# Performance work log

Measured on AMD Instinct MI355X. Metric: run time of the kernel, lower is better.

The kernel has to match this reference:

```python
import jax, jax.numpy as jnp
import numpy as np

N = 100000
E = 1600000
IN_C, HID_C, OUT_C = 128, 256, 40


def sage_conv(x, src, dst, W_l, W_r, b):
    # mean aggregation of source-node features into destination nodes
    msgs = x[src]                                            # [E, d]
    agg = jax.ops.segment_sum(msgs, dst, num_segments=N)     # [N, d]
    deg = jax.ops.segment_sum(jnp.ones((src.shape[0],), x.dtype), dst,
                              num_segments=N)                # [N]
    agg = agg / jnp.clip(deg, 1.0, None)[:, None]
    # out = lin_l(agg) + lin_r(x); weights stored [out, in] like torch
    return agg @ W_l.T + x @ W_r.T + b


def setup_inputs() -> dict:
    key = jax.random.key(0)
    ks = jax.random.split(key, 10)
    s = 0.05
    x = jax.random.normal(ks[0], (N, IN_C), dtype=jnp.float32)
    edge_index = jax.random.randint(ks[1], (2, E), 0, N, dtype=jnp.int64)
    return {
        "x": x,
        "edge_index": edge_index,
        "W_l0": jax.random.normal(ks[2], (HID_C, IN_C), dtype=jnp.float32) * s,
        "W_r0": jax.random.normal(ks[3], (HID_C, IN_C), dtype=jnp.float32) * s,
        "b0": jnp.zeros((HID_C,), jnp.float32),
        "W_l1": jax.random.normal(ks[4], (HID_C, HID_C), dtype=jnp.float32) * s,
        "W_r1": jax.random.normal(ks[5], (HID_C, HID_C), dtype=jnp.float32) * s,
        "b1": jnp.zeros((HID_C,), jnp.float32),
        "W_lo": jax.random.normal(ks[6], (OUT_C, HID_C), dtype=jnp.float32) * s,
        "W_ro": jax.random.normal(ks[7], (OUT_C, HID_C), dtype=jnp.float32) * s,
        "bo": jnp.zeros((OUT_C,), jnp.float32),
    }


def reference(x, edge_index, W_l0, W_r0, b0, W_l1, W_r1, b1, W_lo, W_ro, bo):
    src, dst = edge_index[0], edge_index[1]
    h = jax.nn.relu(sage_conv(x, src, dst, W_l0, W_r0, b0))
    h = jax.nn.relu(sage_conv(h, src, dst, W_l1, W_r1, b1))
    out = sage_conv(h, src, dst, W_lo, W_ro, bo)
    return jax.nn.log_softmax(out, axis=1)
```

## Files before the change

### kernel.cpp

```cpp
#include <hip/hip_runtime.h>
#include <hip/hip_bf16.h>
#include <cstdint>
#include <cstddef>

#define NN   100000
#define NE   1600000
#define HID  256
#define OUTC 40

typedef __attribute__((ext_vector_type(8))) short bf16x8;
typedef __attribute__((ext_vector_type(4))) float f32x4;

static __device__ __forceinline__ ushort f2bf(float f) {
    __hip_bfloat16 h = __float2bfloat16(f);
    return *reinterpret_cast<ushort*>(&h);
}
static __device__ __forceinline__ float bflo(unsigned u) { return __uint_as_float(u << 16); }
static __device__ __forceinline__ float bfhi(unsigned u) { return __uint_as_float(u & 0xffff0000u); }
static __device__ __forceinline__ float ubf(unsigned w, int k) {
    return (float)((w >> (8 * k)) & 255u);
}

__global__ void k_count(const int* __restrict__ dst, int* __restrict__ cnt) {
    int i = blockIdx.x * blockDim.x + threadIdx.x;
    if (i < NE) atomicAdd(&cnt[dst[i]], 1);
}

__global__ void k_blocksum(const int* __restrict__ cnt, int* __restrict__ bsum) {
    __shared__ int s[256];
    int t = threadIdx.x;
    int n = blockIdx.x * 256 + t;
    s[t] = (n < NN) ? cnt[n] : 0;
    __syncthreads();
    for (int off = 128; off; off >>= 1) {
        if (t < off) s[t] += s[t + off];
        __syncthreads();
    }
    if (t == 0) bsum[blockIdx.x] = s[0];
}

__global__ void k_scanblock(const int* __restrict__ bsum, int* __restrict__ boff, int nb) {
    __shared__ int s[512];
    int t = threadIdx.x;
    int v = (t < nb) ? bsum[t] : 0;
    s[t] = v;
    __syncthreads();
    for (int off = 1; off < 512; off <<= 1) {
        int u = (t >= off) ? s[t - off] : 0;
        __syncthreads();
        s[t] += u;
        __syncthreads();
    }
    if (t < nb) boff[t] = s[t] - v;
}

__global__ void k_rowptr(const int* __restrict__ cnt, const int* __restrict__ boff,
                         int* __restrict__ rowptr, int* __restrict__ fillp,
                         float* __restrict__ invd) {
    __shared__ int s[256];
    int t = threadIdx.x;
    int n = blockIdx.x * 256 + t;
    int c = (n < NN) ? cnt[n] : 0;
    s[t] = c;
    __syncthreads();
    for (int off = 1; off < 256; off <<= 1) {
        int u = (t >= off) ? s[t - off] : 0;
        __syncthreads();
        s[t] += u;
        __syncthreads();
    }
    if (n < NN) {
        int excl = boff[blockIdx.x] + s[t] - c;
        rowptr[n] = excl;
        fillp[n]  = excl;
        invd[n]   = 1.0f / (float)(c > 1 ? c : 1);
    }
    if (n == 0) rowptr[NN] = NE;
}

__global__ void k_fill(const int* __restrict__ src, const int* __restrict__ dst,
                       int* __restrict__ fillp, int* __restrict__ colidx) {
    int i = blockIdx.x * blockDim.x + threadIdx.x;
    if (i < NE) {
        int p = atomicAdd(&fillp[dst[i]], 1);
        colidx[p] = src[i];
    }
}

__global__ void k_cvtfrag(const float* __restrict__ W, ushort* __restrict__ dst,
                          int ocreal, int d, int nf) {
    int f = blockIdx.x * 256 + threadIdx.x;
    if (f >= nf) return;
    int lm = f & 15, lk = (f >> 4) & 3;
    int rest = f >> 6;
    int dk = d / 32;
    int kk = rest % dk, cc = rest / dk;
    int row = cc * 16 + lm, col = kk * 32 + lk * 8;
    unsigned q0 = 0, q1 = 0, q2 = 0, q3 = 0;
    if (row < ocreal) {
        const float4* p = (const float4*)(W + (size_t)row * d + col);
        float4 a = p[0], b = p[1];
        q0 = (unsigned)f2bf(a.x) | ((unsigned)f2bf(a.y) << 16);
        q1 = (unsigned)f2bf(a.z) | ((unsigned)f2bf(a.w) << 16);
        q2 = (unsigned)f2bf(b.x) | ((unsigned)f2bf(b.y) << 16);
        q3 = (unsigned)f2bf(b.z) | ((unsigned)f2bf(b.w) << 16);
    }
    *(uint4*)(dst + (size_t)f * 8) = make_uint4(q0, q1, q2, q3);
}

__global__ __launch_bounds__(256) void k_quant_x8(const float* __restrict__ x,
                                                  unsigned char* __restrict__ xq,
                                                  float* __restrict__ sx) {
    int t = threadIdx.x;
    int qw = t >> 4, ql = t & 15;
    int row = blockIdx.x * 16 + qw;
    if (row >= NN) return;
    const float4* p = (const float4*)(x + (size_t)row * 128 + ql * 8);
    float4 a = p[0], b = p[1];
    float v[8] = {a.x, a.y, a.z, a.w, b.x, b.y, b.z, b.w};
    float m = 0.f;
    #pragma unroll
    for (int k = 0; k < 8; ++k) m = fmaxf(m, fabsf(v[k]));
    m = fmaxf(m, __shfl_xor(m, 1));
    m = fmaxf(m, __shfl_xor(m, 2));
    m = fmaxf(m, __shfl_xor(m, 4));
    m = fmaxf(m, __shfl_xor(m, 8));
    float inv = (m > 0.f) ? 127.f / m : 0.f;
    unsigned w0 = 0, w1 = 0;
    #pragma unroll
    for (int k = 0; k < 4; ++k)
        w0 |= ((unsigned)((int)rintf(v[k] * inv) + 128) & 255u) << (8 * k);
    #pragma unroll
    for (int k = 0; k < 4; ++k)
        w1 |= ((unsigned)((int)rintf(v[4 + k] * inv) + 128) & 255u) << (8 * k);
    *(uint2*)(xq + (size_t)row * 128 + ql * 8) = make_uint2(w0, w1);
    if (ql == 0) sx[row] = (m > 0.f) ? m / 127.f : 0.f;
}

__global__ __launch_bounds__(256, 3) void k_layer0(
    const unsigned char* __restrict__ xq, const float* __restrict__ sx,
    const float* __restrict__ xf,
    const ushort* __restrict__ Wl, const ushort* __restrict__ Wr,
    const float* __restrict__ bias, const float* __restrict__ invd,
    const int* __restrict__ rowptr, const int* __restrict__ colidx,
    unsigned char* __restrict__ hq, float* __restrict__ hs)
{
    __shared__ ushort aggS[64 * 128];
    __shared__ int cidxS[2048];
    char* aggSb = (char*)aggS;
    const int t  = threadIdx.x;
    const int r0 = blockIdx.x * 64;
    const int l = t & 63;

    const int ebase = rowptr[r0];
    const int rend  = (r0 + 64 < NN) ? (r0 + 64) : NN;
    const int etot  = rowptr[rend] - ebase;
    const bool inlds = (etot <= 2048);
    if (inlds) {
        for (int i = t; i < etot; i += 256) cidxS[i] = colidx[ebase + i];
    }
    __syncthreads();

    {
        const int gid = t >> 3, li = t & 7;
        const int base = l & ~7;
        for (int rr = gid; rr < 64; rr += 32) {
            const int r = r0 + rr;
            float acc[16];
            #pragma unroll
            for (int k = 0; k < 16; ++k) acc[k] = 0.f;
            float sum_sc = 0.f;
            if (r < NN) {
                const int beg = rowptr[r], end = rowptr[r + 1];
                for (int e = beg; e < end; e += 8) {
                    const int myi = e + li;
                    int se = -1;
                    if (myi < end) se = inlds ? cidxS[myi - ebase] : colidx[myi];
                    float mysc = (se >= 0) ? sx[se] : 0.f;
                    int   sj[8];
                    float sc[8];
                    uint4 u[8];
                    #pragma unroll
                    for (int j = 0; j < 8; ++j) sj[j] = __shfl(se, base + j);
                    #pragma unroll
                    for (int j = 0; j < 8; ++j) sc[j] = __shfl(mysc, base + j);
                    #pragma unroll
                    for (int j = 0; j < 8; ++j) {
                        u[j] = (sj[j] >= 0)
                            ? *(const uint4*)(xq + (((unsigned)sj[j]) << 7) + (li << 4))
                            : make_uint4(0u, 0u, 0u, 0u);
                    }
                    #pragma unroll
                    for (int j = 0; j < 8; ++j) {
                        #pragma unroll
                        for (int wi = 0; wi < 4; ++wi) {
                            unsigned w = (&u[j].x)[wi];
                            acc[wi*4+0] = fmaf(sc[j], ubf(w, 0), acc[wi*4+0]);
                            acc[wi*4+1] = fmaf(sc[j], ubf(w, 1), acc[wi*4+1]);
                            acc[wi*4+2] = fmaf(sc[j], ubf(w, 2), acc[wi*4+2]);
                            acc[wi*4+3] = fmaf(sc[j], ubf(w, 3), acc[wi*4+3]);
                        }
                        sum_sc += sc[j];
                    }
                }
                const float iv = invd[r];
                #pragma unroll
                for (int k = 0; k < 16; ++k) acc[k] = (acc[k] - 128.f * sum_sc) * iv;
            }
            #pragma unroll
            for (int gg = 0; gg < 2; ++gg) {
                unsigned q0 = (unsigned)f2bf(acc[gg*8+0]) | ((unsigned)f2bf(acc[gg*8+1]) << 16);
                unsigned q1 = (unsigned)f2bf(acc[gg*8+2]) | ((unsigned)f2bf(acc[gg*8+3]) << 16);
                unsigned q2 = (unsigned)f2bf(acc[gg*8+4]) | ((unsigned)f2bf(acc[gg*8+5]) << 16);
                unsigned q3 = (unsigned)f2bf(acc[gg*8+6]) | ((unsigned)f2bf(acc[gg*8+7]) << 16);
                int g  = li * 2 + gg;
                int gs = g ^ (rr & 7);
                *(uint4*)(aggSb + (size_t)rr * 256 + (gs << 4)) = make_uint4(q0, q1, q2, q3);
            }
        }
    }
    __syncthreads();

    const int w = t >> 6, lm = l & 15, lk = l >> 4;
    const int rr = w * 16 + lm;
    const int rg = r0 + rr;

    bf16x8 ax[4];
    #pragma unroll
    for (int kk = 0; kk < 4; ++kk) {
        bf16x8 v;
        if (rg < NN) {
            const float4* p = (const float4*)(xf + (size_t)rg * 128 + kk * 32 + lk * 8);
            float4 f0 = p[0], f1 = p[1];
            v[0] = (short)f2bf(f0.x); v[1] = (short)f2bf(f0.y);
            v[2] = (short)f2bf(f0.z); v[3] = (short)f2bf(f0.w);
            v[4] = (short)f2bf(f1.x); v[5] = (short)f2bf(f1.y);
            v[6] = (short)f2bf(f1.z); v[7] = (short)f2bf(f1.w);
        } else v = (bf16x8)(short)0;
        ax[kk] = v;
    }

    f32x4 acc[16];
    #pragma unroll
    for (int cc = 0; cc < 16; ++cc) acc[cc] = {0.f, 0.f, 0.f, 0.f};

    #pragma unroll
    for (int kk = 0; kk < 4; ++kk) {
        int g  = kk * 4 + lk;
        int gs = g ^ (rr & 7);
        bf16x8 a_agg = *(const bf16x8*)(aggSb + (size_t)rr * 256 + (gs << 4));
        #pragma unroll
        for (int cc = 0; cc < 16; ++cc) {
            const size_t wf = ((size_t)(cc * 4 + kk) * 64 + l) * 8;
            bf16x8 bl = *(const bf16x8*)(Wl + wf);
            bf16x8 br = *(const bf16x8*)(Wr + wf);
            acc[cc] = __builtin_amdgcn_mfma_f32_16x16x32_bf16(a_agg,  bl, acc[cc], 0, 0, 0);
            acc[cc] = __builtin_amdgcn_mfma_f32_16x16x32_bf16(ax[kk], br, acc[cc], 0, 0, 0);
        }
    }

    float vmax[4] = {0.f, 0.f, 0.f, 0.f};
    #pragma unroll
    for (int cc = 0; cc < 16; ++cc) {
        const float bv = bias[cc * 16 + lm];
        #pragma unroll
        for (int i = 0; i < 4; ++i) {
            float v = fmaxf(acc[cc][i] + bv, 0.f);
            acc[cc][i] = v;
            vmax[i] = fmaxf(vmax[i], v);
        }
    }
    #pragma unroll
    for (int i = 0; i < 4; ++i) {
        vmax[i] = fmaxf(vmax[i], __shfl_xor(vmax[i], 1));
        vmax[i] = fmaxf(vmax[i], __shfl_xor(vmax[i], 2));
        vmax[i] = fmaxf(vmax[i], __shfl_xor(vmax[i], 4));
        vmax[i] = fmaxf(vmax[i], __shfl_xor(vmax[i], 8));
    }
    float invq[4];
    #pragma unroll
    for (int i = 0; i < 4; ++i) invq[i] = (vmax[i] > 0.f) ? 255.f / vmax[i] : 0.f;
    const int ob = r0 + w * 16 + lk * 4;
    if (lm == 0) {
        #pragma unroll
        for (int i = 0; i < 4; ++i)
            if (ob + i < NN) hs[ob + i] = vmax[i] / 255.f;
    }
    #pragma unroll
    for (int cc = 0; cc < 16; ++cc) {
        #pragma unroll
        for (int i = 0; i < 4; ++i) {
            if (ob + i < NN)
                hq[(size_t)(ob + i) * 256 + cc * 16 + lm] =
                    (unsigned char)(int)rintf(acc[cc][i] * invq[i]);
        }
    }
}

__global__ __launch_bounds__(256, 3) void k_layer1(
    const unsigned char* __restrict__ hq, const float* __restrict__ hs,
    const ushort* __restrict__ Wl, const ushort* __restrict__ Wr,
    const float* __restrict__ bias,
    const ushort* __restrict__ wlo, const ushort* __restrict__ wro,
    const float* __restrict__ bo,
    const float* __restrict__ invd,
    const int* __restrict__ rowptr, const int* __restrict__ colidx,
    unsigned char* __restrict__ qq, float* __restrict__ sq, float* __restrict__ rbuf)
{
    __shared__ ushort aggS[64 * 256];
    __shared__ int cidxS[2048];
    char* aggSb = (char*)aggS;
    const int t  = threadIdx.x;
    const int r0 = blockIdx.x * 64;
    const int l = t & 63;

    const int ebase = rowptr[r0];
    const int rend  = (r0 + 64 < NN) ? (r0 + 64) : NN;
    const int etot  = rowptr[rend] - ebase;
    const bool inlds = (etot <= 2048);
    if (inlds) {
        for (int i = t; i < etot; i += 256) cidxS[i] = colidx[ebase + i];
    }
    __syncthreads();

    {
        const int gid = t >> 4, li = t & 15;
        const int base = l & ~15;
        for (int rr = gid; rr < 64; rr += 16) {
            const int r = r0 + rr;
            float acc[16];
            #pragma unroll
            for (int k = 0; k < 16; ++k) acc[k] = 0.f;
            if (r < NN) {
                const int beg = rowptr[r], end = rowptr[r + 1];
                for (int e = beg; e < end; e += 8) {
                    const int myi = e + (li & 7);
                    int se = -1;
                    if (myi < end) se = inlds ? cidxS[myi - ebase] : colidx[myi];
                    float mysc = (se >= 0) ? hs[se] : 0.f;
                    int   sj[8];
                    float sc[8];
                    uint4 u[8];
                    #pragma unroll
                    for (int j = 0; j < 8; ++j) sj[j] = __shfl(se, base + j);
                    #pragma unroll
                    for (int j = 0; j < 8; ++j) sc[j] = __shfl(mysc, base + j);
                    #pragma unroll
                    for (int j = 0; j < 8; ++j) {
                        u[j] = (sj[j] >= 0)
                            ? *(const uint4*)(hq + (((unsigned)sj[j]) << 8) + (li << 4))
                            : make_uint4(0u, 0u, 0u, 0u);
                    }
                    #pragma unroll
                    for (int j = 0; j < 8; ++j) {
                        #pragma unroll
                        for (int wi = 0; wi < 4; ++wi) {
                            unsigned w = (&u[j].x)[wi];
                            acc[wi*4+0] = fmaf(sc[j], ubf(w, 0), acc[wi*4+0]);
                            acc[wi*4+1] = fmaf(sc[j], ubf(w, 1), acc[wi*4+1]);
                            acc[wi*4+2] = fmaf(sc[j], ubf(w, 2), acc[wi*4+2]);
                            acc[wi*4+3] = fmaf(sc[j], ubf(w, 3), acc[wi*4+3]);
                        }
                    }
                }
                const float iv = invd[r];
                #pragma unroll
                for (int k = 0; k < 16; ++k) acc[k] *= iv;
            }
            #pragma unroll
            for (int gg = 0; gg < 2; ++gg) {
                unsigned q0 = (unsigned)f2bf(acc[gg*8+0]) | ((unsigned)f2bf(acc[gg*8+1]) << 16);
                unsigned q1 = (unsigned)f2bf(acc[gg*8+2]) | ((unsigned)f2bf(acc[gg*8+3]) << 16);
                unsigned q2 = (unsigned)f2bf(acc[gg*8+4]) | ((unsigned)f2bf(acc[gg*8+5]) << 16);
                unsigned q3 = (unsigned)f2bf(acc[gg*8+6]) | ((unsigned)f2bf(acc[gg*8+7]) << 16);
                int g  = li * 2 + gg;
                int gs = g ^ (rr & 7);
                *(uint4*)(aggSb + (size_t)rr * 512 + (gs << 4)) = make_uint4(q0, q1, q2, q3);
            }
        }
    }
    __syncthreads();

    const int w = t >> 6, lm = l & 15, lk = l >> 4;
    const int rr = w * 16 + lm;
    const int rg = r0 + rr;

    bf16x8 ax[8];
    {
        const float sr = (rg < NN) ? hs[rg] : 0.f;
        #pragma unroll
        for (int kk = 0; kk < 8; ++kk) {
            uint2 uq = (rg < NN)
                ? *(const uint2*)(hq + (((unsigned)rg) << 8) + kk * 32 + lk * 8)
                : make_uint2(0u, 0u);
            bf16x8 v;
            v[0] = (short)f2bf(sr * ubf(uq.x, 0));
            v[1] = (short)f2bf(sr * ubf(uq.x, 1));
            v[2] = (short)f2bf(sr * ubf(uq.x, 2));
            v[3] = (short)f2bf(sr * ubf(uq.x, 3));
            v[4] = (short)f2bf(sr * ubf(uq.y, 0));
            v[5] = (short)f2bf(sr * ubf(uq.y, 1));
            v[6] = (short)f2bf(sr * ubf(uq.y, 2));
            v[7] = (short)f2bf(sr * ubf(uq.y, 3));
            ax[kk] = v;
        }
    }

    f32x4 acc[16];
    #pragma unroll
    for (int cc = 0; cc < 16; ++cc) acc[cc] = {0.f, 0.f, 0.f, 0.f};

    #pragma unroll
    for (int kk = 0; kk < 8; ++kk) {
        int g  = kk * 4 + lk;
        int gs = g ^ (rr & 7);
        bf16x8 a_agg = *(const bf16x8*)(aggSb + (size_t)rr * 512 + (gs << 4));
        #pragma unroll
        for (int cc = 0; cc < 16; ++cc) {
            const size_t wf = ((size_t)(cc * 8 + kk) * 64 + l) * 8;
            bf16x8 bl = *(const bf16x8*)(Wl + wf);
            bf16x8 br = *(const bf16x8*)(Wr + wf);
            acc[cc] = __builtin_amdgcn_mfma_f32_16x16x32_bf16(a_agg,  bl, acc[cc], 0, 0, 0);
            acc[cc] = __builtin_amdgcn_mfma_f32_16x16x32_bf16(ax[kk], br, acc[cc], 0, 0, 0);
        }
    }

    #pragma unroll
    for (int cc = 0; cc < 16; ++cc) {
        const int c = cc * 16 + lm;
        const float bv = bias[c];
        #pragma unroll
        for (int i = 0; i < 4; ++i) {
            float v = fmaxf(acc[cc][i] + bv, 0.f);
            int row = w * 16 + lk * 4 + i;
            int g = c >> 3;
            int gs = g ^ (row & 7);
            *(ushort*)(aggSb + (size_t)row * 512 + (gs << 4) + ((c & 7) << 1)) = f2bf(v);
        }
    }
    __syncthreads();

    f32x4 aq[3], ar[3];
    #pragma unroll
    for (int cc = 0; cc < 3; ++cc) { aq[cc] = {0.f,0.f,0.f,0.f}; ar[cc] = {0.f,0.f,0.f,0.f}; }

    const int prow = w * 16 + lm;
    #pragma unroll
    for (int kk = 0; kk < 8; ++kk) {
        int g  = kk * 4 + lk;
        int gs = g ^ (prow & 7);
        bf16x8 a = *(const bf16x8*)(aggSb + (size_t)prow * 512 + (gs << 4));
        #pragma unroll
        for (int cc = 0; cc < 3; ++cc) {
            const size_t wf = ((size_t)(cc * 8 + kk) * 64 + l) * 8;
            bf16x8 bl = *(const bf16x8*)(wlo + wf);
            bf16x8 br = *(const bf16x8*)(wro + wf);
            aq[cc] = __builtin_amdgcn_mfma_f32_16x16x32_bf16(a, bl, aq[cc], 0, 0, 0);
            ar[cc] = __builtin_amdgcn_mfma_f32_16x16x32_bf16(a, br, ar[cc], 0, 0, 0);
        }
    }

    #pragma unroll
    for (int i = 0; i < 4; ++i) {
        const int orow = r0 + w * 16 + lk * 4 + i;
        if (orow >= NN) continue;
        float m = 0.f;
        #pragma unroll
        for (int cc = 0; cc < 3; ++cc) {
            const int c = cc * 16 + lm;
            if (c < OUTC) m = fmaxf(m, fabsf(aq[cc][i]));
        }
        m = fmaxf(m, __shfl_xor(m, 1));
        m = fmaxf(m, __shfl_xor(m, 2));
        m = fmaxf(m, __shfl_xor(m, 4));
        m = fmaxf(m, __shfl_xor(m, 8));
        const float inv = (m > 0.f) ? 127.f / m : 0.f;
        #pragma unroll
        for (int cc = 0; cc < 3; ++cc) {
            const int c = cc * 16 + lm;
            int code = (c < OUTC) ? (int)rintf(aq[cc][i] * inv) : 0;
            qq[(size_t)orow * 64 + c] = (unsigned char)(code + 128);
            rbuf[(size_t)orow * 64 + c] = (c < OUTC) ? (ar[cc][i] + bo[c]) : 0.f;
        }
        qq[(size_t)orow * 64 + 48 + lm] = (unsigned char)128;
        rbuf[(size_t)orow * 64 + 48 + lm] = 0.f;
        if (lm == 0) sq[orow] = m / 127.f;
    }
}

__global__ __launch_bounds__(256) void k_final(
    const unsigned char* __restrict__ qq, const float* __restrict__ sq,
    const float* __restrict__ rbuf, const float* __restrict__ invd,
    const int* __restrict__ rowptr, const int* __restrict__ colidx,
    float* __restrict__ out)
{
    __shared__ int cidxS[2048];
    const int t = threadIdx.x;
    const int g = t >> 2, li = t & 3;
    const int r0 = blockIdx.x * 64;
    const int row = r0 + g;
    const int l = t & 63;
    const int base = l & ~3;

    const int ebase = rowptr[r0];
    const int rend  = (r0 + 64 < NN) ? (r0 + 64) : NN;
    const int etot  = rowptr[rend] - ebase;
    const bool inlds = (etot <= 2048);
    if (inlds) {
        for (int i = t; i < etot; i += 256) cidxS[i] = colidx[ebase + i];
    }
    __syncthreads();
    if (row >= NN) return;

    float acc[16];
    #pragma unroll
    for (int k = 0; k < 16; ++k) acc[k] = 0.f;
    float sum_sc = 0.f;

    const int beg = rowptr[row], end = rowptr[row + 1];
    for (int e = beg; e < end; e += 8) {
        const int m0 = e + li, m1 = e + 4 + li;
        int se0 = -1, se1 = -1;
        if (m0 < end) se0 = inlds ? cidxS[m0 - ebase] : colidx[m0];
        if (m1 < end) se1 = inlds ? cidxS[m1 - ebase] : colidx[m1];
        float ms0 = (se0 >= 0) ? sq[se0] : 0.f;
        float ms1 = (se1 >= 0) ? sq[se1] : 0.f;
        int   sj[8];
        float sc[8];
        uint4 u[8];
        #pragma unroll
        for (int j = 0; j < 4; ++j) { sj[j] = __shfl(se0, base + j); sc[j] = __shfl(ms0, base + j); }
        #pragma unroll
        for (int j = 4; j < 8; ++j) { sj[j] = __shfl(se1, base + j - 4); sc[j] = __shfl(ms1, base + j - 4); }
        #pragma unroll
        for (int j = 0; j < 8; ++j) {
            u[j] = (sj[j] >= 0)
                ? *(const uint4*)(qq + (((unsigned)sj[j]) << 6) + (li << 4))
                : make_uint4(0u, 0u, 0u, 0u);
        }
        #pragma unroll
        for (int j = 0; j < 8; ++j) {
            #pragma unroll
            for (int wi = 0; wi < 4; ++wi) {
                unsigned w = (&u[j].x)[wi];
                acc[wi*4+0] = fmaf(sc[j], ubf(w, 0), acc[wi*4+0]);
                acc[wi*4+1] = fmaf(sc[j], ubf(w, 1), acc[wi*4+1]);
                acc[wi*4+2] = fmaf(sc[j], ubf(w, 2), acc[wi*4+2]);
                acc[wi*4+3] = fmaf(sc[j], ubf(w, 3), acc[wi*4+3]);
            }
            sum_sc += sc[j];
        }
    }

    const float iv = invd[row];
    const float4* rp = (const float4*)(rbuf + (size_t)row * 64 + li * 16);
    float v[16];
    #pragma unroll
    for (int ch = 0; ch < 4; ++ch) {
        float4 rv = rp[ch];
        v[ch*4+0] = (acc[ch*4+0] - 128.f * sum_sc) * iv + rv.x;
        v[ch*4+1] = (acc[ch*4+1] - 128.f * sum_sc) * iv + rv.y;
        v[ch*4+2] = (acc[ch*4+2] - 128.f * sum_sc) * iv + rv.z;
        v[ch*4+3] = (acc[ch*4+3] - 128.f * sum_sc) * iv + rv.w;
    }
    #pragma unroll
    for (int k = 0; k < 16; ++k)
        if (li * 16 + k >= OUTC) v[k] = -INFINITY;

    float m = v[0];
    #pragma unroll
    for (int k = 1; k < 16; ++k) m = fmaxf(m, v[k]);
    m = fmaxf(m, __shfl_xor(m, 1));
    m = fmaxf(m, __shfl_xor(m, 2));

    float s = 0.f;
    #pragma unroll
    for (int k = 0; k < 16; ++k)
        if (li * 16 + k < OUTC) s += __expf(v[k] - m);
    s += __shfl_xor(s, 1);
    s += __shfl_xor(s, 2);
    const float ls = __logf(s);

    #pragma unroll
    for (int ch = 0; ch < 4; ++ch) {
        const int c = li * 16 + ch * 4;
        if (c < OUTC) {
            float4 o;
            o.x = v[ch*4+0] - m - ls;
            o.y = v[ch*4+1] - m - ls;
            o.z = v[ch*4+2] - m - ls;
            o.w = v[ch*4+3] - m - ls;
            *(float4*)(out + (size_t)row * OUTC + c) = o;
        }
    }
}

extern "C" void kernel_launch(void* const* d_in, const int* in_sizes, int n_in,
                              void* d_out, int out_size, void* d_ws, size_t ws_size,
                              hipStream_t stream) {
    const float* x   = (const float*)d_in[0];
    const int*   ei  = (const int*)d_in[1];
    const int*   src = ei;
    const int*   dst = ei + NE;
    const float* Wl0 = (const float*)d_in[2];
    const float* Wr0 = (const float*)d_in[3];
    const float* b0  = (const float*)d_in[4];
    const float* Wl1 = (const float*)d_in[5];
    const float* Wr1 = (const float*)d_in[6];
    const float* b1  = (const float*)d_in[7];
    const float* Wlo = (const float*)d_in[8];
    const float* Wro = (const float*)d_in[9];
    const float* bo  = (const float*)d_in[10];
    float* out = (float*)d_out;

    char* ws = (char*)d_ws;
    const size_t MB = 1 << 20;
    float*         invd   = (float*)(ws + 0);
    int*           rowptr = (int*)(ws + MB / 2);
    int*           cnt    = (int*)(ws + MB);
    int*           fillp  = (int*)(ws + MB + MB / 2);
    int*           bsum   = (int*)(ws + 2 * MB);
    int*           boff   = (int*)(ws + 2 * MB + MB / 4);
    float*         sx     = (float*)(ws + 2 * MB + MB / 2);
    float*         s0     = (float*)(ws + 3 * MB);
    float*         sq     = (float*)(ws + 3 * MB + MB / 2);
    ushort*        Wb     = (ushort*)(ws + 4 * MB);
    int*           colidx = (int*)(ws + 4 * MB + MB / 2);
    unsigned char* xq8    = (unsigned char*)(ws + 11 * MB);
    unsigned char* qq     = (unsigned char*)(ws + 11 * MB);
    unsigned char* h0q    = (unsigned char*)(ws + 24 * MB);
    float*         rbuf   = (float*)(ws + 50 * MB);

    ushort* wl0 = Wb;
    ushort* wr0 = Wb + 32768;
    ushort* wl1 = Wb + 65536;
    ushort* wr1 = Wb + 131072;
    ushort* wlo = Wb + 196608;
    ushort* wro = Wb + 208896;

    hipMemsetAsync(cnt, 0, NN * sizeof(int), stream);
    k_count<<<(NE + 255) / 256, 256, 0, stream>>>(dst, cnt);
    const int NB = (NN + 255) / 256;
    k_blocksum<<<NB, 256, 0, stream>>>(cnt, bsum);
    k_scanblock<<<1, 512, 0, stream>>>(bsum, boff, NB);
    k_rowptr<<<NB, 256, 0, stream>>>(cnt, boff, rowptr, fillp, invd);
    k_fill<<<(NE + 255) / 256, 256, 0, stream>>>(src, dst, fillp, colidx);

    k_cvtfrag<<<16, 256, 0, stream>>>(Wl0, wl0, 256, 128, 4096);
    k_cvtfrag<<<16, 256, 0, stream>>>(Wr0, wr0, 256, 128, 4096);
    k_cvtfrag<<<32, 256, 0, stream>>>(Wl1, wl1, 256, 256, 8192);
    k_cvtfrag<<<32, 256, 0, stream>>>(Wr1, wr1, 256, 256, 8192);
    k_cvtfrag<<<6,  256, 0, stream>>>(Wlo, wlo, 40, 256, 1536);
    k_cvtfrag<<<6,  256, 0, stream>>>(Wro, wro, 40, 256, 1536);
    k_quant_x8<<<(NN + 15) / 16, 256, 0, stream>>>(x, xq8, sx);

    const int GB = (NN + 63) / 64;
    k_layer0<<<GB, 256, 0, stream>>>(xq8, sx, x, wl0, wr0, b0, invd, rowptr, colidx, h0q, s0);
    k_layer1<<<GB, 256, 0, stream>>>(h0q, s0, wl1, wr1, b1, wlo, wro, bo,
                                     invd, rowptr, colidx, qq, sq, rbuf);
    k_final<<<GB, 256, 0, stream>>>(qq, sq, rbuf, invd, rowptr, colidx, out);
}
```

Measured before the change: 533.5 us.

## Split layer1 output projection into separate kernel and raise occupancy bounds

The layer-1 kernel no longer runs the final 40-column projection. It now writes the bf16 hidden activations to a global buffer, and a new k_premul kernel reads them back to do the output projection and quantization. Layer1 also loops over output column tiles one at a time with a single accumulator instead of holding 16, and both layer kernels raise launch bounds from 3 to 4 blocks per CU to cut register pressure and raise occupancy. The cost is an extra kernel launch plus a round trip of about 51 MB of bf16 activations through memory, and the column loop reloads the weight fragments in sequence.

```diff
diff --git a/kernel.cpp b/kernel.cpp
--- a/kernel.cpp
+++ b/kernel.cpp
@@ -137,7 +137,7 @@
     if (ql == 0) sx[row] = (m > 0.f) ? m / 127.f : 0.f;
 }
 
-__global__ __launch_bounds__(256, 3) void k_layer0(
+__global__ __launch_bounds__(256, 4) void k_layer0(
     const unsigned char* __restrict__ xq, const float* __restrict__ sx,
     const float* __restrict__ xf,
     const ushort* __restrict__ Wl, const ushort* __restrict__ Wr,
@@ -239,23 +239,27 @@
         } else v = (bf16x8)(short)0;
         ax[kk] = v;
     }
-
-    f32x4 acc[16];
-    #pragma unroll
-    for (int cc = 0; cc < 16; ++cc) acc[cc] = {0.f, 0.f, 0.f, 0.f};
-
+    bf16x8 agg_reg[4];
     #pragma unroll
     for (int kk = 0; kk < 4; ++kk) {
         int g  = kk * 4 + lk;
         int gs = g ^ (rr & 7);
-        bf16x8 a_agg = *(const bf16x8*)(aggSb + (size_t)rr * 256 + (gs << 4));
+        agg_reg[kk] = *(const bf16x8*)(aggSb + (size_t)rr * 256 + (gs << 4));
+    }
+
+    f32x4 acc[16];
+    #pragma unroll
+    for (int cc = 0; cc < 16; ++cc) acc[cc] = {0.f, 0.f, 0.f, 0.f};
+
+    #pragma unroll
+    for (int kk = 0; kk < 4; ++kk) {
         #pragma unroll
         for (int cc = 0; cc < 16; ++cc) {
             const size_t wf = ((size_t)(cc * 4 + kk) * 64 + l) * 8;
             bf16x8 bl = *(const bf16x8*)(Wl + wf);
             bf16x8 br = *(const bf16x8*)(Wr + wf);
-            acc[cc] = __builtin_amdgcn_mfma_f32_16x16x32_bf16(a_agg,  bl, acc[cc], 0, 0, 0);
-            acc[cc] = __builtin_amdgcn_mfma_f32_16x16x32_bf16(ax[kk], br, acc[cc], 0, 0, 0);
+            acc[cc] = __builtin_amdgcn_mfma_f32_16x16x32_bf16(agg_reg[kk], bl, acc[cc], 0, 0, 0);
+            acc[cc] = __builtin_amdgcn_mfma_f32_16x16x32_bf16(ax[kk],      br, acc[cc], 0, 0, 0);
         }
     }
 
@@ -297,15 +301,12 @@
     }
 }
 
-__global__ __launch_bounds__(256, 3) void k_layer1(
+__global__ __launch_bounds__(256, 4) void k_layer1(
     const unsigned char* __restrict__ hq, const float* __restrict__ hs,
     const ushort* __restrict__ Wl, const ushort* __restrict__ Wr,
-    const float* __restrict__ bias,
-    const ushort* __restrict__ wlo, const ushort* __restrict__ wro,
-    const float* __restrict__ bo,
-    const float* __restrict__ invd,
+    const float* __restrict__ bias, const float* __restrict__ invd,
     const int* __restrict__ rowptr, const int* __restrict__ colidx,
-    unsigned char* __restrict__ qq, float* __restrict__ sq, float* __restrict__ rbuf)
+    ushort* __restrict__ hout)
 {
     __shared__ ushort aggS[64 * 256];
     __shared__ int cidxS[2048];
@@ -405,51 +406,57 @@
             ax[kk] = v;
         }
     }
-
-    f32x4 acc[16];
-    #pragma unroll
-    for (int cc = 0; cc < 16; ++cc) acc[cc] = {0.f, 0.f, 0.f, 0.f};
-
+    bf16x8 agg_reg[8];
     #pragma unroll
     for (int kk = 0; kk < 8; ++kk) {
         int g  = kk * 4 + lk;
         int gs = g ^ (rr & 7);
-        bf16x8 a_agg = *(const bf16x8*)(aggSb + (size_t)rr * 512 + (gs << 4));
-        #pragma unroll
-        for (int cc = 0; cc < 16; ++cc) {
+        agg_reg[kk] = *(const bf16x8*)(aggSb + (size_t)rr * 512 + (gs << 4));
+    }
+
+    for (int cc = 0; cc < 16; ++cc) {
+        const int c = cc * 16 + lm;
+        f32x4 acc = {0.f, 0.f, 0.f, 0.f};
+        #pragma unroll
+        for (int kk = 0; kk < 8; ++kk) {
             const size_t wf = ((size_t)(cc * 8 + kk) * 64 + l) * 8;
             bf16x8 bl = *(const bf16x8*)(Wl + wf);
             bf16x8 br = *(const bf16x8*)(Wr + wf);
-            acc[cc] = __builtin_amdgcn_mfma_f32_16x16x32_bf16(a_agg,  bl, acc[cc], 0, 0, 0);
-            acc[cc] = __builtin_amdgcn_mfma_f32_16x16x32_bf16(ax[kk], br, acc[cc], 0, 0, 0);
-        }
-    }
-
-    #pragma unroll
-    for (int cc = 0; cc < 16; ++cc) {
-        const int c = cc * 16 + lm;
+            acc = __builtin_amdgcn_mfma_f32_16x16x32_bf16(agg_reg[kk], bl, acc, 0, 0, 0);
+            acc = __builtin_amdgcn_mfma_f32_16x16x32_bf16(ax[kk],      br, acc, 0, 0, 0);
+        }
         const float bv = bias[c];
         #pragma unroll
         for (int i = 0; i < 4; ++i) {
-            float v = fmaxf(acc[cc][i] + bv, 0.f);
-            int row = w * 16 + lk * 4 + i;
-            int g = c >> 3;
-            int gs = g ^ (row & 7);
-            *(ushort*)(aggSb + (size_t)row * 512 + (gs << 4) + ((c & 7) << 1)) = f2bf(v);
-        }
-    }
-    __syncthreads();
+            const int orow = r0 + w * 16 + lk * 4 + i;
+            if (orow < NN) {
+                float v = fmaxf(acc[i] + bv, 0.f);
+                hout[(size_t)orow * HID + c] = f2bf(v);
+            }
+        }
+    }
+}
+
+__global__ __launch_bounds__(256, 4) void k_premul(
+    const ushort* __restrict__ h1, const ushort* __restrict__ wlo,
+    const ushort* __restrict__ wro, const float* __restrict__ bo,
+    unsigned char* __restrict__ qq, float* __restrict__ sq, float* __restrict__ rbuf)
+{
+    const int t = threadIdx.x;
+    const int r0 = blockIdx.x * 64;
+    const int w = t >> 6, l = t & 63, lm = l & 15, lk = l >> 4;
+    const int rr = w * 16 + lm;
+    const int rg = r0 + rr;
 
     f32x4 aq[3], ar[3];
     #pragma unroll
     for (int cc = 0; cc < 3; ++cc) { aq[cc] = {0.f,0.f,0.f,0.f}; ar[cc] = {0.f,0.f,0.f,0.f}; }
 
-    const int prow = w * 16 + lm;
     #pragma unroll
     for (int kk = 0; kk < 8; ++kk) {
-        int g  = kk * 4 + lk;
-        int gs = g ^ (prow & 7);
-        bf16x8 a = *(const bf16x8*)(aggSb + (size_t)prow * 512 + (gs << 4));
+        bf16x8 a = (rg < NN)
+            ? *(const bf16x8*)(h1 + (size_t)rg * 256 + kk * 32 + lk * 8)
+            : (bf16x8)(short)0;
         #pragma unroll
         for (int cc = 0; cc < 3; ++cc) {
             const size_t wf = ((size_t)(cc * 8 + kk) * 64 + l) * 8;
@@ -629,7 +636,8 @@
     unsigned char* xq8    = (unsigned char*)(ws + 11 * MB);
     unsigned char* qq     = (unsigned char*)(ws + 11 * MB);
     unsigned char* h0q    = (unsigned char*)(ws + 24 * MB);
-    float*         rbuf   = (float*)(ws + 50 * MB);
+    float*         rbuf   = (float*)(ws + 24 * MB);
+    ushort*        h1     = (ushort*)(ws + 50 * MB);
 
     ushort* wl0 = Wb;
     ushort* wr0 = Wb + 32768;
@@ -656,7 +664,7 @@
 
     const int GB = (NN + 63) / 64;
     k_layer0<<<GB, 256, 0, stream>>>(xq8, sx, x, wl0, wr0, b0, invd, rowptr, colidx, h0q, s0);
-    k_layer1<<<GB, 256, 0, stream>>>(h0q, s0, wl1, wr1, b1, wlo, wro, bo,
-                                     invd, rowptr, colidx, qq, sq, rbuf);
+    k_layer1<<<GB, 256, 0, stream>>>(h0q, s0, wl1, wr1, b1, invd, rowptr, colidx, h1);
+    k_premul<<<GB, 256, 0, stream>>>(h1, wlo, wro, bo, qq, sq, rbuf);
     k_final<<<GB, 256, 0, stream>>>(qq, sq, rbuf, invd, rowptr, colidx, out);
 }
```

Result: faster. 509.5 us, median of 2 (-4.5%).
